# Optimization experiments

Measured on AMD Instinct MI355X. Metric: run time of the kernel, lower is better.

The kernel has to match this reference:

```python
import jax, jax.numpy as jnp
import numpy as np

B, T, D = 64, 128, 512  # batch, seq_len, d_model == memory_dim


def setup_inputs() -> dict:
    key = jax.random.key(0)
    ks = jax.random.split(key, 14)
    bound = 1.0 / np.sqrt(D)  # nn.Linear / kaiming_uniform(a=sqrt(5)) bound for fan_in=D
    u = lambda k, shape: jax.random.uniform(k, shape, jnp.float32, -bound, bound)
    return {
        "x": jax.random.normal(ks[0], (B, T, D), jnp.float32),
        "W_Q": u(ks[1], (D, D)),
        "W_K": u(ks[2], (D, D)),
        "W_V": u(ks[3], (D, D)),
        "theta_w": u(ks[4], (1, D)), "theta_b": u(ks[5], (1,)),
        "eta_w": u(ks[6], (1, D)), "eta_b": u(ks[7], (1,)),
        "alpha_w": u(ks[8], (1, D)), "alpha_b": u(ks[9], (1,)),
        "W1": u(ks[10], (D, D)), "b1": u(ks[11], (D,)),
        "W2": u(ks[12], (D, D)), "b2": u(ks[13], (D,)),
    }


def _run(x, W_Q, W_K, W_V, theta_w, theta_b, eta_w, eta_b, alpha_w, alpha_b,
         W1, b1, W2, b2):
    LO, HI = 1e-10, 1e10  # loss clamp range (grad passes through strictly inside)
    Bn, Tn, Dn = x.shape
    N = Bn * Dn  # mse_loss 'mean' normalizer over (batch, memory_dim)

    def step(carry, x_t):  # x_t: (B, D)
        cW1, cb1, cW2, cb2, M1w, M1b, M2w, M2b = carry
        # read path: q -> 2-layer memory MLP (relu, then linear)
        q = x_t @ W_Q.T
        mem = jax.nn.relu(q @ cW1.T + cb1) @ cW2.T + cb2
        # per-step scalar gates: mean over batch of sigmoid(proj(x_t))
        theta = jnp.mean(jax.nn.sigmoid(x_t @ theta_w.T + theta_b))
        eta = jnp.mean(jax.nn.sigmoid(x_t @ eta_w.T + eta_b))
        alpha = jnp.mean(jax.nn.sigmoid(x_t @ alpha_w.T + alpha_b))
        # write path: grad of clamped mean MSE( MLP(k), v ) wrt memory weights
        k = x_t @ W_K.T
        v = x_t @ W_V.T
        h_pre = k @ cW1.T + cb1
        h = jax.nn.relu(h_pre)
        out = h @ cW2.T + cb2
        diff = out - v
        loss = jnp.mean(diff * diff)
        pt = jnp.where((loss >= LO) & (loss <= HI), 1.0, 0.0)  # clamp passthrough
        dout = (pt * 2.0 / N) * diff                            # (B, D)
        gW2 = dout.T @ h
        gb2 = dout.sum(0)
        dpre = jnp.where(h_pre > 0, dout @ cW2, 0.0)
        gW1 = dpre.T @ k
        gb1 = dpre.sum(0)
        # momentum + weight decay update
        M1w = eta * M1w - theta * gW1
        M1b = eta * M1b - theta * gb1
        M2w = eta * M2w - theta * gW2
        M2b = eta * M2b - theta * gb2
        nW1 = (1.0 - alpha) * cW1 + M1w
        nb1 = (1.0 - alpha) * cb1 + M1b
        nW2 = (1.0 - alpha) * cW2 + M2w
        nb2 = (1.0 - alpha) * cb2 + M2b
        return (nW1, nb1, nW2, nb2, M1w, M1b, M2w, M2b), mem

    carry0 = (W1, b1, W2, b2,
              jnp.zeros_like(W1), jnp.zeros_like(b1),
              jnp.zeros_like(W2), jnp.zeros_like(b2))
    _, mem_seq = jax.lax.scan(step, carry0, jnp.swapaxes(x, 0, 1))  # (T, B, D)
    return jnp.swapaxes(mem_seq, 0, 1)  # (B, T, D)


def reference(x, W_Q, W_K, W_V, theta_w, theta_b, eta_w, eta_b, alpha_w, alpha_b,
              W1, b1, W2, b2):
    outputs = _run(x, W_Q, W_K, W_V, theta_w, theta_b, eta_w, eta_b,
                   alpha_w, alpha_b, W1, b1, W2, b2)
    # original returns (outputs, memory_outputs), which are identical tensors
    return (outputs, outputs)
```

## Files before the change

### kernel.cpp

```cpp
#include <hip/hip_runtime.h>
#include <stdint.h>


typedef __attribute__((ext_vector_type(8))) short short8;
typedef __attribute__((ext_vector_type(4))) float floatx4;

#define GBLK 16
#define SC_AGENT __HIP_MEMORY_SCOPE_AGENT

__device__ inline floatx4 mfma_bf16(short8 a, short8 b, floatx4 c) {
  return __builtin_amdgcn_mfma_f32_16x16x32_bf16(a, b, c, 0, 0, 0);
}
__device__ inline unsigned short f2bf(float f) {
  unsigned u = __float_as_uint(f);
  u += 0x7fffu + ((u >> 16) & 1u);
  return (unsigned short)(u >> 16);
}
__device__ inline float bf2f(unsigned short h) {
  return __uint_as_float(((unsigned)h) << 16);
}
__device__ inline short8 ldbf8(const unsigned short* p) {
  return *reinterpret_cast<const short8*>(p);
}
__device__ inline void st2_sc(unsigned short* p, unsigned short v) {
  __hip_atomic_store(p, v, __ATOMIC_RELAXED, SC_AGENT);
}
__device__ inline void st8_sc(unsigned short* p, unsigned long long v) {
  __hip_atomic_store(reinterpret_cast<unsigned long long*>(p), v,
                     __ATOMIC_RELAXED, SC_AGENT);
}
__device__ inline short8 ld16_sc(const unsigned short* p) {
  union { unsigned long long u[2]; short8 s; } c;
  c.u[0] = __hip_atomic_load(reinterpret_cast<const unsigned long long*>(p),
                             __ATOMIC_RELAXED, SC_AGENT);
  c.u[1] = __hip_atomic_load(reinterpret_cast<const unsigned long long*>(p + 4),
                             __ATOMIC_RELAXED, SC_AGENT);
  return c.s;
}
__device__ inline unsigned long long pack4(const unsigned short* p) {
  return (unsigned long long)p[0] | ((unsigned long long)p[1] << 16) |
         ((unsigned long long)p[2] << 32) | ((unsigned long long)p[3] << 48);
}
__device__ inline short8 pack8(const float* p) {
  float4 a = *reinterpret_cast<const float4*>(p);
  float4 b = *reinterpret_cast<const float4*>(p + 4);
  short8 r;
  r[0] = (short)f2bf(a.x); r[1] = (short)f2bf(a.y);
  r[2] = (short)f2bf(a.z); r[3] = (short)f2bf(a.w);
  r[4] = (short)f2bf(b.x); r[5] = (short)f2bf(b.y);
  r[6] = (short)f2bf(b.z); r[7] = (short)f2bf(b.w);
  return r;
}

__device__ inline void gridbar(unsigned* ctr, unsigned& ep) {
  __syncthreads();
  if (threadIdx.x == 0) {
    __hip_atomic_fetch_add(ctr, 1u, __ATOMIC_RELAXED, SC_AGENT);
    const unsigned target = (ep + 1u) * GBLK;
    while (__hip_atomic_load(ctr, __ATOMIC_RELAXED, SC_AGENT) < target)
      __builtin_amdgcn_s_sleep(1);
  }
  ++ep;
  __syncthreads();
}

__global__ __launch_bounds__(256) void qkv_kernel(
    const float* __restrict__ x, const float* __restrict__ WQ,
    const float* __restrict__ WK, const float* __restrict__ WV,
    unsigned short* __restrict__ qb, unsigned short* __restrict__ kb,
    unsigned short* __restrict__ vb, unsigned short* __restrict__ kbT) {
  const int tid = threadIdx.x;
  const int lane = tid & 63, w = tid >> 6;
  const int quad = lane >> 4, l16 = lane & 15;
  const int Mbase = blockIdx.x * 128;
  const int Nbase = blockIdx.y * 128;
  const int z = blockIdx.z;
  const float* W = (z == 0) ? WQ : (z == 1) ? WK : WV;
  unsigned short* dst = (z == 0) ? qb : (z == 1) ? kb : vb;

  floatx4 acc[2][8];
  for (int a = 0; a < 2; ++a)
    for (int n = 0; n < 8; ++n) acc[a][n] = (floatx4){0.f, 0.f, 0.f, 0.f};

  const int r0 = Mbase + w * 32 + l16;
  for (int ks = 0; ks < 16; ++ks) {
    const int k0 = ks * 32 + quad * 8;
    short8 a0 = pack8(x + (size_t)r0 * 512 + k0);
    short8 a1 = pack8(x + (size_t)(r0 + 16) * 512 + k0);
    for (int n = 0; n < 8; ++n) {
      short8 b = pack8(W + (size_t)(Nbase + n * 16 + l16) * 512 + k0);
      acc[0][n] = mfma_bf16(a0, b, acc[0][n]);
      acc[1][n] = mfma_bf16(a1, b, acc[1][n]);
    }
  }
  for (int tm = 0; tm < 2; ++tm)
    for (int n = 0; n < 8; ++n)
      for (int rr = 0; rr < 4; ++rr) {
        int row = Mbase + w * 32 + tm * 16 + quad * 4 + rr;
        int col = Nbase + n * 16 + l16;
        int b = row >> 7, t = row & 127;
        unsigned short val = f2bf(acc[tm][n][rr]);
        dst[((size_t)(t * 64 + b) << 9) + col] = val;
        if (z == 1) kbT[((size_t)(t * 512 + col) << 6) + b] = val;
      }
}

__global__ __launch_bounds__(256) void gates_kernel(
    const float* __restrict__ x,
    const float* __restrict__ tw, const float* __restrict__ tb,
    const float* __restrict__ ew, const float* __restrict__ eb,
    const float* __restrict__ aw, const float* __restrict__ ab,
    float* __restrict__ gates, float* __restrict__ lossAcc,
    unsigned* __restrict__ ctr) {
  const int t = blockIdx.x, tid = threadIdx.x;
  __shared__ float red[192];
  if (tid < 192) {
    int g = tid >> 6, b = tid & 63;
    const float* wr = (g == 0) ? tw : (g == 1) ? ew : aw;
    float bias = (g == 0) ? tb[0] : (g == 1) ? eb[0] : ab[0];
    const float* xr = x + ((size_t)b * 128 + t) * 512;
    float s = 0.f;
    for (int i = 0; i < 512; i += 4) {
      float4 xv = *reinterpret_cast<const float4*>(xr + i);
      float4 wv = *reinterpret_cast<const float4*>(wr + i);
      s += xv.x * wv.x + xv.y * wv.y + xv.z * wv.z + xv.w * wv.w;
    }
    red[tid] = 1.f / (1.f + expf(-(s + bias)));
  }
  if (tid == 192) lossAcc[t] = 0.f;
  if (tid == 193 && t == 0) *ctr = 0u;
  __syncthreads();
  if (tid < 3) {
    float s = 0.f;
    for (int i = 0; i < 64; ++i) s += red[tid * 64 + i];
    gates[tid * 128 + t] = s * (1.f / 64.f);
  }
}

__global__ __launch_bounds__(512, 1) void scan_kernel(
    const unsigned short* __restrict__ qb, const unsigned short* __restrict__ kb,
    const unsigned short* __restrict__ vb, const unsigned short* __restrict__ kbT,
    const float* __restrict__ gates, float* lossAcc, unsigned* ctr,
    const float* __restrict__ inW1, const float* __restrict__ inb1,
    const float* __restrict__ inW2, const float* __restrict__ inb2,
    unsigned short* W2T, unsigned short* RcG, unsigned short* hT,
    unsigned short* dout_rm, float* __restrict__ out) {
  __shared__ unsigned short sW1[32 * 520];
  __shared__ unsigned short sW2[32 * 520];
  __shared__ unsigned short sdt[32 * 72];
  __shared__ unsigned short sdp[32 * 72];
  __shared__ unsigned short shl[32 * 72];
  __shared__ float b1loc[32], b2loc[32], mb1[32], mb2[32];

  const int tid = threadIdx.x, bid = blockIdx.x;
  const int lane = tid & 63, w = tid >> 6;
  const int quad = lane >> 4, l16 = lane & 15;
  const int J = bid * 32;
  const int mt = w & 1, ng = w >> 1;
  const int mtc = w & 3, ntc = w >> 2;
  unsigned ep = 0;

  float w1s[32], m1s[32], w2s[32], m2s[32];
#pragma unroll
  for (int g = 0; g < 8; ++g)
#pragma unroll
    for (int rr = 0; rr < 4; ++rr) {
      const int jl = mt * 16 + quad * 4 + rr;
      const int l = (ng * 8 + g) * 16 + l16;
      const int si = g * 4 + rr;
      const size_t gi = (size_t)(J + jl) * 512 + l;
      float a = inW1[gi]; w1s[si] = a; m1s[si] = 0.f; sW1[jl * 520 + l] = f2bf(a);
      float b = inW2[gi]; w2s[si] = b; m2s[si] = 0.f; sW2[jl * 520 + l] = f2bf(b);
    }
  if (tid < 32) {
    b1loc[tid] = inb1[J + tid]; mb1[tid] = 0.f;
    b2loc[tid] = inb2[J + tid]; mb2[tid] = 0.f;
  }
  __syncthreads();
  {
    const int l = tid;
    unsigned short tmp[32];
#pragma unroll
    for (int c = 0; c < 32; ++c) tmp[c] = sW2[c * 520 + l];
    unsigned short* dstp = W2T + (size_t)l * 512 + J;
#pragma unroll
    for (int s4 = 0; s4 < 8; ++s4) st8_sc(dstp + s4 * 4, pack4(tmp + s4 * 4));
  }

  for (int t = 0; t < 128; ++t) {
    const int par = t & 1, nxt = par ^ 1;
    const float th = gates[t], et = gates[128 + t], al = gates[256 + t];
    const float oma = 1.f - al;
    const unsigned short* qt = qb + ((size_t)t << 15);
    const unsigned short* kt = kb + ((size_t)t << 15);
    const unsigned short* vt = vb + ((size_t)t << 15);
    const unsigned short* ktT = kbT + ((size_t)t << 15);
    unsigned short* hTp = hT + par * 32768;
    const unsigned short* w2tp = W2T + (size_t)par * 262144;
    unsigned short* w2tn = W2T + (size_t)nxt * 262144;

    {
      const int row = w * 16 + l16;
      const unsigned short* arow = (row < 64) ? (qt + (size_t)row * 512)
                                              : (kt + (size_t)(row - 64) * 512);
      floatx4 a0 = {0.f,0.f,0.f,0.f}, a1 = {0.f,0.f,0.f,0.f};
#pragma unroll
      for (int half = 0; half < 2; ++half) {
        short8 af[8];
#pragma unroll
        for (int ks = 0; ks < 8; ++ks)
          af[ks] = ldbf8(arow + (half * 8 + ks) * 32 + quad * 8);
#pragma unroll
        for (int ks = 0; ks < 8; ++ks) {
          const int k0 = (half * 8 + ks) * 32 + quad * 8;
          short8 b0 = *reinterpret_cast<const short8*>(&sW1[l16 * 520 + k0]);
          short8 b1f = *reinterpret_cast<const short8*>(&sW1[(16 + l16) * 520 + k0]);
          a0 = mfma_bf16(af[ks], b0, a0);
          a1 = mfma_bf16(af[ks], b1f, a1);
        }
      }
      const float bi0 = b1loc[l16], bi1 = b1loc[16 + l16];
#pragma unroll
      for (int rr = 0; rr < 4; ++rr) {
        const int orow = w * 16 + quad * 4 + rr;
        float v0 = fmaxf(a0[rr] + bi0, 0.f);
        float v1 = fmaxf(a1[rr] + bi1, 0.f);
        unsigned short h0 = f2bf(v0), h1 = f2bf(v1);
        st2_sc(RcG + (size_t)orow * 512 + J + l16, h0);
        st2_sc(RcG + (size_t)orow * 512 + J + 16 + l16, h1);
        if (orow >= 64) {
          const int i = orow - 64;
          st2_sc(hTp + (size_t)(J + l16) * 64 + i, h0);
          st2_sc(hTp + (size_t)(J + 16 + l16) * 64 + i, h1);
          shl[l16 * 72 + i] = h0;
          shl[(16 + l16) * 72 + i] = h1;
        }
      }
    }
    gridbar(ctr, ep);

    {
      const int row = w * 16 + l16;
      const unsigned short* arow = RcG + (size_t)row * 512;
      floatx4 a0 = {0.f,0.f,0.f,0.f}, a1 = {0.f,0.f,0.f,0.f};
#pragma unroll
      for (int half = 0; half < 2; ++half) {
        short8 af[8];
#pragma unroll
        for (int ks = 0; ks < 8; ++ks)
          af[ks] = ld16_sc(arow + (half * 8 + ks) * 32 + quad * 8);
#pragma unroll
        for (int ks = 0; ks < 8; ++ks) {
          const int k0 = (half * 8 + ks) * 32 + quad * 8;
          short8 b0 = *reinterpret_cast<const short8*>(&sW2[l16 * 520 + k0]);
          short8 b1f = *reinterpret_cast<const short8*>(&sW2[(16 + l16) * 520 + k0]);
          a0 = mfma_bf16(af[ks], b0, a0);
          a1 = mfma_bf16(af[ks], b1f, a1);
        }
      }
      const float bi0 = b2loc[l16], bi1 = b2loc[16 + l16];
      float lossp = 0.f;
#pragma unroll
      for (int rr = 0; rr < 4; ++rr) {
        const int orow = w * 16 + quad * 4 + rr;
        float o0 = a0[rr] + bi0, o1 = a1[rr] + bi1;
        if (orow < 64) {
          size_t o = ((size_t)orow * 128 + t) * 512;
          out[o + J + l16] = o0;
          out[o + J + 16 + l16] = o1;
          out[4194304 + o + J + l16] = o0;
          out[4194304 + o + J + 16 + l16] = o1;
        } else {
          const int i = orow - 64;
          float d0 = o0 - bf2f(vt[(size_t)i * 512 + J + l16]);
          float d1 = o1 - bf2f(vt[(size_t)i * 512 + J + 16 + l16]);
          lossp += d0 * d0 + d1 * d1;
          unsigned short q0 = f2bf(6.103515625e-5f * d0);
          unsigned short q1 = f2bf(6.103515625e-5f * d1);
          st2_sc(dout_rm + (size_t)i * 512 + J + l16, q0);
          st2_sc(dout_rm + (size_t)i * 512 + J + 16 + l16, q1);
          sdt[l16 * 72 + i] = q0;
          sdt[(16 + l16) * 72 + i] = q1;
        }
      }
      if (w >= 4) {
        for (int off = 32; off > 0; off >>= 1) lossp += __shfl_down(lossp, off);
        if (lane == 0)
          __hip_atomic_fetch_add(lossAcc + t, lossp, __ATOMIC_RELAXED, SC_AGENT);
      }
    }
    gridbar(ctr, ep);

    const float loss =
        __hip_atomic_load(lossAcc + t, __ATOMIC_RELAXED, SC_AGENT) * (1.f / 32768.f);
    const float pt = (loss >= 1e-10f && loss <= 1e10f) ? 1.f : 0.f;

    {
      const unsigned short* arow = dout_rm + (size_t)(mtc * 16 + l16) * 512;
      const unsigned short* brow = w2tp + (size_t)(J + ntc * 16 + l16) * 512;
      floatx4 acc = {0.f,0.f,0.f,0.f};
#pragma unroll
      for (int half = 0; half < 2; ++half) {
        short8 afr[8], bfr[8];
#pragma unroll
        for (int ks = 0; ks < 8; ++ks) {
          const int k0 = (half * 8 + ks) * 32 + quad * 8;
          afr[ks] = ld16_sc(arow + k0);
          bfr[ks] = ld16_sc(brow + k0);
        }
#pragma unroll
        for (int ks = 0; ks < 8; ++ks) acc = mfma_bf16(afr[ks], bfr[ks], acc);
      }
#pragma unroll
      for (int rr = 0; rr < 4; ++rr) {
        const int i = mtc * 16 + quad * 4 + rr;
        const int jl = ntc * 16 + l16;
        unsigned short hb = shl[jl * 72 + i];
        sdp[jl * 72 + i] = (hb != 0) ? f2bf(acc[rr]) : (unsigned short)0;
      }
    }
    __syncthreads();

    {
      floatx4 acc1[8];
#pragma unroll
      for (int g = 0; g < 8; ++g) acc1[g] = (floatx4){0.f,0.f,0.f,0.f};
#pragma unroll
      for (int half = 0; half < 2; ++half) {
        short8 bfr[2][4];
#pragma unroll
        for (int ks = 0; ks < 2; ++ks)
#pragma unroll
          for (int g = 0; g < 4; ++g) {
            const int l = (ng * 8 + half * 4 + g) * 16 + l16;
            bfr[ks][g] = ldbf8(ktT + (size_t)l * 64 + ks * 32 + quad * 8);
          }
#pragma unroll
        for (int ks = 0; ks < 2; ++ks) {
          short8 af = *reinterpret_cast<const short8*>(
              &sdp[(mt * 16 + l16) * 72 + ks * 32 + quad * 8]);
#pragma unroll
          for (int g = 0; g < 4; ++g)
            acc1[half * 4 + g] = mfma_bf16(af, bfr[ks][g], acc1[half * 4 + g]);
        }
      }
#pragma unroll
      for (int g = 0; g < 8; ++g)
#pragma unroll
        for (int rr = 0; rr < 4; ++rr) {
          const int jl = mt * 16 + quad * 4 + rr;
          const int l = (ng * 8 + g) * 16 + l16;
          const int si = g * 4 + rr;
          float m = et * m1s[si] - th * (pt * acc1[g][rr]);
          float wv = oma * w1s[si] + m;
          m1s[si] = m; w1s[si] = wv;
          sW1[jl * 520 + l] = f2bf(wv);
        }
      if (tid < 32) {
        float s = 0.f;
        for (int i = 0; i < 64; ++i) s += bf2f(sdp[tid * 72 + i]);
        float m = et * mb1[tid] - th * (pt * s);
        float bv = oma * b1loc[tid] + m;
        mb1[tid] = m; b1loc[tid] = bv;
      }
    }

    {
      floatx4 acc2[8];
#pragma unroll
      for (int g = 0; g < 8; ++g) acc2[g] = (floatx4){0.f,0.f,0.f,0.f};
#pragma unroll
      for (int half = 0; half < 2; ++half) {
        short8 bfr[2][4];
#pragma unroll
        for (int ks = 0; ks < 2; ++ks)
#pragma unroll
          for (int g = 0; g < 4; ++g) {
            const int l = (ng * 8 + half * 4 + g) * 16 + l16;
            bfr[ks][g] = ld16_sc(hTp + (size_t)l * 64 + ks * 32 + quad * 8);
          }
#pragma unroll
        for (int ks = 0; ks < 2; ++ks) {
          short8 af = *reinterpret_cast<const short8*>(
              &sdt[(mt * 16 + l16) * 72 + ks * 32 + quad * 8]);
#pragma unroll
          for (int g = 0; g < 4; ++g)
            acc2[half * 4 + g] = mfma_bf16(af, bfr[ks][g], acc2[half * 4 + g]);
        }
      }
#pragma unroll
      for (int g = 0; g < 8; ++g)
#pragma unroll
        for (int rr = 0; rr < 4; ++rr) {
          const int jl = mt * 16 + quad * 4 + rr;
          const int l = (ng * 8 + g) * 16 + l16;
          const int si = g * 4 + rr;
          float m = et * m2s[si] - th * (pt * acc2[g][rr]);
          float wv = oma * w2s[si] + m;
          m2s[si] = m; w2s[si] = wv;
          sW2[jl * 520 + l] = f2bf(wv);
        }
      if (tid < 32) {
        float s = 0.f;
        for (int i = 0; i < 64; ++i) s += bf2f(sdt[tid * 72 + i]);
        float m = et * mb2[tid] - th * (pt * s);
        float bv = oma * b2loc[tid] + m;
        mb2[tid] = m; b2loc[tid] = bv;
      }
    }
    __syncthreads();

    {
      const int l = tid;
      unsigned short tmp[32];
#pragma unroll
      for (int c = 0; c < 32; ++c) tmp[c] = sW2[c * 520 + l];
      unsigned short* dstp = w2tn + (size_t)l * 512 + J;
#pragma unroll
      for (int s4 = 0; s4 < 8; ++s4) st8_sc(dstp + s4 * 4, pack4(tmp + s4 * 4));
    }
    __syncthreads();
  }
}

extern "C" void kernel_launch(void* const* d_in, const int* in_sizes, int n_in,
                              void* d_out, int out_size, void* d_ws, size_t ws_size,
                              hipStream_t stream) {
  const float* x  = (const float*)d_in[0];
  const float* WQ = (const float*)d_in[1];
  const float* WK = (const float*)d_in[2];
  const float* WV = (const float*)d_in[3];
  const float* tw = (const float*)d_in[4];
  const float* tb = (const float*)d_in[5];
  const float* ew = (const float*)d_in[6];
  const float* eb = (const float*)d_in[7];
  const float* aw = (const float*)d_in[8];
  const float* ab = (const float*)d_in[9];
  const float* W1 = (const float*)d_in[10];
  const float* b1 = (const float*)d_in[11];
  const float* W2 = (const float*)d_in[12];
  const float* b2 = (const float*)d_in[13];
  float* out = (float*)d_out;

  char* ws = (char*)d_ws;
  size_t off = 0;
  auto alloc = [&](size_t b) {
    char* p = ws + off;
    off = (off + b + 255) & ~(size_t)255;
    return p;
  };
  unsigned short* qb   = (unsigned short*)alloc(8388608);
  unsigned short* kb   = (unsigned short*)alloc(8388608);
  unsigned short* vb   = (unsigned short*)alloc(8388608);
  unsigned short* kbT  = (unsigned short*)alloc(8388608);
  float* gates   = (float*)alloc(1536);
  float* lossAcc = (float*)alloc(512);
  unsigned* ctr  = (unsigned*)alloc(256);
  unsigned short* W2T  = (unsigned short*)alloc(1048576);
  unsigned short* RcG  = (unsigned short*)alloc(131072);
  unsigned short* hT   = (unsigned short*)alloc(131072);
  unsigned short* dout_rm = (unsigned short*)alloc(65536);
  (void)in_sizes; (void)n_in; (void)out_size; (void)ws_size;

  qkv_kernel<<<dim3(64, 4, 3), 256, 0, stream>>>(x, WQ, WK, WV, qb, kb, vb, kbT);
  gates_kernel<<<dim3(128), 256, 0, stream>>>(x, tw, tb, ew, eb, aw, ab,
                                              gates, lossAcc, ctr);
  scan_kernel<<<dim3(GBLK), 512, 0, stream>>>(
      qb, kb, vb, kbT, gates, lossAcc, ctr,
      W1, b1, W2, b2,
      W2T, RcG, hT, dout_rm, out);
}
```

Baseline: 7.756 ms.

## Stage cross-block global stores through LDS as 16-byte coherent vector writes

Replaces the scattered 2-byte and 8-byte atomic-scoped global stores of RcG, hT, dout, W2T and the output rows with LDS staging, followed by coalesced 16-byte global_store_dwordx4 with sc0 sc1 cache bits. An explicit vmcnt(0) wait before each grid barrier keeps cross-block visibility. A transposed LDS copy of W2 is maintained so the W2T write-out is contiguous. This cuts the number of store instructions and uncoalesced traffic in the serial scan, at the cost of extra LDS, extra __syncthreads, and reliance on inline asm for coherence; launch_bounds is also changed.

```diff
diff --git a/kernel.cpp b/kernel.cpp
--- a/kernel.cpp
+++ b/kernel.cpp
@@ -22,12 +22,12 @@
 __device__ inline short8 ldbf8(const unsigned short* p) {
   return *reinterpret_cast<const short8*>(p);
 }
-__device__ inline void st2_sc(unsigned short* p, unsigned short v) {
-  __hip_atomic_store(p, v, __ATOMIC_RELAXED, SC_AGENT);
-}
-__device__ inline void st8_sc(unsigned short* p, unsigned long long v) {
-  __hip_atomic_store(reinterpret_cast<unsigned long long*>(p), v,
-                     __ATOMIC_RELAXED, SC_AGENT);
+__device__ inline void stg16_sc(unsigned short* p, short8 v) {
+  asm volatile("global_store_dwordx4 %0, %1, off sc0 sc1"
+               :: "v"(p), "v"(v) : "memory");
+}
+__device__ inline void vmwait() {
+  asm volatile("s_waitcnt vmcnt(0)" ::: "memory");
 }
 __device__ inline short8 ld16_sc(const unsigned short* p) {
   union { unsigned long long u[2]; short8 s; } c;
@@ -36,10 +36,6 @@
   c.u[1] = __hip_atomic_load(reinterpret_cast<const unsigned long long*>(p + 4),
                              __ATOMIC_RELAXED, SC_AGENT);
   return c.s;
-}
-__device__ inline unsigned long long pack4(const unsigned short* p) {
-  return (unsigned long long)p[0] | ((unsigned long long)p[1] << 16) |
-         ((unsigned long long)p[2] << 32) | ((unsigned long long)p[3] << 48);
 }
 __device__ inline short8 pack8(const float* p) {
   float4 a = *reinterpret_cast<const float4*>(p);
@@ -53,6 +49,7 @@
 }
 
 __device__ inline void gridbar(unsigned* ctr, unsigned& ep) {
+  vmwait();
   __syncthreads();
   if (threadIdx.x == 0) {
     __hip_atomic_fetch_add(ctr, 1u, __ATOMIC_RELAXED, SC_AGENT);
@@ -137,7 +134,7 @@
   }
 }
 
-__global__ __launch_bounds__(512, 1) void scan_kernel(
+__global__ __launch_bounds__(512, 2) void scan_kernel(
     const unsigned short* __restrict__ qb, const unsigned short* __restrict__ kb,
     const unsigned short* __restrict__ vb, const unsigned short* __restrict__ kbT,
     const float* __restrict__ gates, float* lossAcc, unsigned* ctr,
@@ -147,9 +144,13 @@
     unsigned short* dout_rm, float* __restrict__ out) {
   __shared__ unsigned short sW1[32 * 520];
   __shared__ unsigned short sW2[32 * 520];
+  __shared__ unsigned short sWT[512 * 40];
+  __shared__ unsigned short shl[32 * 72];
   __shared__ unsigned short sdt[32 * 72];
   __shared__ unsigned short sdp[32 * 72];
-  __shared__ unsigned short shl[32 * 72];
+  __shared__ unsigned short sStA[128 * 32];
+  __shared__ unsigned short sDR[64 * 32];
+  __shared__ float sOutF[64 * 32];
   __shared__ float b1loc[32], b2loc[32], mb1[32], mb2[32];
 
   const int tid = threadIdx.x, bid = blockIdx.x;
@@ -162,7 +163,8 @@
 
   float w1s[32], m1s[32], w2s[32], m2s[32];
 #pragma unroll
-  for (int g = 0; g < 8; ++g)
+  for (int g = 0; g < 8; ++g) {
+    unsigned short tp[4];
 #pragma unroll
     for (int rr = 0; rr < 4; ++rr) {
       const int jl = mt * 16 + quad * 4 + rr;
@@ -170,21 +172,27 @@
       const int si = g * 4 + rr;
       const size_t gi = (size_t)(J + jl) * 512 + l;
       float a = inW1[gi]; w1s[si] = a; m1s[si] = 0.f; sW1[jl * 520 + l] = f2bf(a);
-      float b = inW2[gi]; w2s[si] = b; m2s[si] = 0.f; sW2[jl * 520 + l] = f2bf(b);
-    }
+      float b = inW2[gi]; w2s[si] = b; m2s[si] = 0.f;
+      unsigned short bb = f2bf(b);
+      sW2[jl * 520 + l] = bb; tp[rr] = bb;
+    }
+    const int l = (ng * 8 + g) * 16 + l16;
+    *reinterpret_cast<unsigned long long*>(&sWT[l * 40 + mt * 16 + quad * 4]) =
+        (unsigned long long)tp[0] | ((unsigned long long)tp[1] << 16) |
+        ((unsigned long long)tp[2] << 32) | ((unsigned long long)tp[3] << 48);
+  }
   if (tid < 32) {
     b1loc[tid] = inb1[J + tid]; mb1[tid] = 0.f;
     b2loc[tid] = inb2[J + tid]; mb2[tid] = 0.f;
   }
   __syncthreads();
   {
-    const int l = tid;
-    unsigned short tmp[32];
-#pragma unroll
-    for (int c = 0; c < 32; ++c) tmp[c] = sW2[c * 520 + l];
-    unsigned short* dstp = W2T + (size_t)l * 512 + J;
-#pragma unroll
-    for (int s4 = 0; s4 < 8; ++s4) st8_sc(dstp + s4 * 4, pack4(tmp + s4 * 4));
+#pragma unroll
+    for (int ii = 0; ii < 4; ++ii) {
+      const int r = w * 64 + ii * 16 + (lane >> 2), c = lane & 3;
+      short8 v = *reinterpret_cast<const short8*>(&sWT[r * 40 + c * 8]);
+      stg16_sc(W2T + (size_t)r * 512 + J + c * 8, v);
+    }
   }
 
   for (int t = 0; t < 128; ++t) {
@@ -226,15 +234,24 @@
         float v0 = fmaxf(a0[rr] + bi0, 0.f);
         float v1 = fmaxf(a1[rr] + bi1, 0.f);
         unsigned short h0 = f2bf(v0), h1 = f2bf(v1);
-        st2_sc(RcG + (size_t)orow * 512 + J + l16, h0);
-        st2_sc(RcG + (size_t)orow * 512 + J + 16 + l16, h1);
+        sStA[orow * 32 + l16] = h0;
+        sStA[orow * 32 + 16 + l16] = h1;
         if (orow >= 64) {
           const int i = orow - 64;
-          st2_sc(hTp + (size_t)(J + l16) * 64 + i, h0);
-          st2_sc(hTp + (size_t)(J + 16 + l16) * 64 + i, h1);
           shl[l16 * 72 + i] = h0;
           shl[(16 + l16) * 72 + i] = h1;
         }
+      }
+      __syncthreads();
+      {
+        const int r = w * 16 + (lane >> 2), c = lane & 3;
+        short8 v = *reinterpret_cast<const short8*>(&sStA[r * 32 + c * 8]);
+        stg16_sc(RcG + (size_t)r * 512 + J + c * 8, v);
+      }
+      if (w < 4) {
+        const int r = w * 8 + (lane >> 3), c = lane & 7;
+        short8 v = *reinterpret_cast<const short8*>(&shl[r * 72 + c * 8]);
+        stg16_sc(hTp + (size_t)(J + r) * 64 + c * 8, v);
       }
     }
     gridbar(ctr, ep);
@@ -265,11 +282,8 @@
         const int orow = w * 16 + quad * 4 + rr;
         float o0 = a0[rr] + bi0, o1 = a1[rr] + bi1;
         if (orow < 64) {
-          size_t o = ((size_t)orow * 128 + t) * 512;
-          out[o + J + l16] = o0;
-          out[o + J + 16 + l16] = o1;
-          out[4194304 + o + J + l16] = o0;
-          out[4194304 + o + J + 16 + l16] = o1;
+          sOutF[orow * 32 + l16] = o0;
+          sOutF[orow * 32 + 16 + l16] = o1;
         } else {
           const int i = orow - 64;
           float d0 = o0 - bf2f(vt[(size_t)i * 512 + J + l16]);
@@ -277,11 +291,25 @@
           lossp += d0 * d0 + d1 * d1;
           unsigned short q0 = f2bf(6.103515625e-5f * d0);
           unsigned short q1 = f2bf(6.103515625e-5f * d1);
-          st2_sc(dout_rm + (size_t)i * 512 + J + l16, q0);
-          st2_sc(dout_rm + (size_t)i * 512 + J + 16 + l16, q1);
+          sDR[i * 32 + l16] = q0;
+          sDR[i * 32 + 16 + l16] = q1;
           sdt[l16 * 72 + i] = q0;
           sdt[(16 + l16) * 72 + i] = q1;
         }
+      }
+      if (w < 4) {
+#pragma unroll
+        for (int ii = 0; ii < 2; ++ii) {
+          const int r = w * 16 + ii * 8 + (lane >> 3), c = lane & 7;
+          float4 v = *reinterpret_cast<const float4*>(&sOutF[r * 32 + c * 4]);
+          float* o0p = out + ((size_t)r * 128 + t) * 512 + J + c * 4;
+          *reinterpret_cast<float4*>(o0p) = v;
+          *reinterpret_cast<float4*>(o0p + 4194304) = v;
+        }
+      } else {
+        const int r = (w - 4) * 16 + (lane >> 2), c = lane & 3;
+        short8 v = *reinterpret_cast<const short8*>(&sDR[r * 32 + c * 8]);
+        stg16_sc(dout_rm + (size_t)r * 512 + J + c * 8, v);
       }
       if (w >= 4) {
         for (int off = 32; off > 0; off >>= 1) lossp += __shfl_down(lossp, off);
@@ -389,7 +417,8 @@
         }
       }
 #pragma unroll
-      for (int g = 0; g < 8; ++g)
+      for (int g = 0; g < 8; ++g) {
+        unsigned short tp[4];
 #pragma unroll
         for (int rr = 0; rr < 4; ++rr) {
           const int jl = mt * 16 + quad * 4 + rr;
@@ -398,8 +427,14 @@
           float m = et * m2s[si] - th * (pt * acc2[g][rr]);
           float wv = oma * w2s[si] + m;
           m2s[si] = m; w2s[si] = wv;
-          sW2[jl * 520 + l] = f2bf(wv);
-        }
+          unsigned short bb = f2bf(wv);
+          sW2[jl * 520 + l] = bb; tp[rr] = bb;
+        }
+        const int l = (ng * 8 + g) * 16 + l16;
+        *reinterpret_cast<unsigned long long*>(&sWT[l * 40 + mt * 16 + quad * 4]) =
+            (unsigned long long)tp[0] | ((unsigned long long)tp[1] << 16) |
+            ((unsigned long long)tp[2] << 32) | ((unsigned long long)tp[3] << 48);
+      }
       if (tid < 32) {
         float s = 0.f;
         for (int i = 0; i < 64; ++i) s += bf2f(sdt[tid * 72 + i]);
@@ -411,16 +446,16 @@
     __syncthreads();
 
     {
-      const int l = tid;
-      unsigned short tmp[32];
-#pragma unroll
-      for (int c = 0; c < 32; ++c) tmp[c] = sW2[c * 520 + l];
-      unsigned short* dstp = w2tn + (size_t)l * 512 + J;
-#pragma unroll
-      for (int s4 = 0; s4 < 8; ++s4) st8_sc(dstp + s4 * 4, pack4(tmp + s4 * 4));
+#pragma unroll
+      for (int ii = 0; ii < 4; ++ii) {
+        const int r = w * 64 + ii * 16 + (lane >> 2), c = lane & 3;
+        short8 v = *reinterpret_cast<const short8*>(&sWT[r * 40 + c * 8]);
+        stg16_sc(w2tn + (size_t)r * 512 + J + c * 8, v);
+      }
     }
     __syncthreads();
   }
+  vmwait();
 }
 
 extern "C" void kernel_launch(void* const* d_in, const int* in_sizes, int n_in,
```

New measurement: 6.699 ms. -13.6%, faster.
